# Kernel tuning notes

Hardware: AMD Instinct MI355X
Metric: run time of the kernel (lower is better)

Reference implementation:

```python
import jax, jax.numpy as jnp
import numpy as np

K = 2            # negative:positive edge ratio (init arg k)
N_NODES = 4096
N_EDGES = 8192
FEAT = 64


def setup_inputs() -> dict:
    key = jax.random.key(0)
    k1, k2, k3 = jax.random.split(key, 3)
    node_feature = jax.random.normal(k1, (N_NODES, FEAT), dtype=jnp.float32)
    edge_src = jax.random.randint(k2, (N_EDGES,), 0, N_NODES, dtype=jnp.int32)
    edge_dst = jax.random.randint(k3, (N_EDGES,), 0, N_NODES, dtype=jnp.int32)
    return {"node_feature": node_feature, "edge_src": edge_src, "edge_dst": edge_dst}


def reference(node_feature, edge_src, edge_dst):
    E = edge_src.shape[0]
    N = node_feature.shape[0]
    # [E, E] pairwise mask: candidate column j is valid for row i iff
    # dst[j] != dst[i] and dst[j] != src[i]
    valid = (edge_dst[:, None] != edge_dst[None, :]) & (edge_src[:, None] != edge_dst[None, :])
    # unsorted_segment_min over rows grouped by edge_src -> [N, E]
    segmin = jax.ops.segment_min(valid.astype(jnp.int8), edge_src, num_segments=N)
    # gather back per edge -> [E, E], flatten
    m = segmin[edge_src].reshape(-1).astype(bool)  # [E*E]
    num_negatives = jnp.sum(m)
    ratio = num_negatives // E                      # integer ratio as in TF code
    keep_prob = (K / ratio).astype(jnp.float32)
    u = jax.random.uniform(jax.random.key(42), (E * E,), dtype=jnp.float32)
    keep = m & (u < keep_prob)
    # fixed-size (jit-friendly) stand-in for tf.boolean_mask: expected count is K*E;
    # pad/truncate to exactly K*E kept flat indices (fill_value=0 pads).
    idx = jnp.nonzero(keep, size=K * E, fill_value=0)[0]
    rows = idx // E
    cols = idx % E
    edge_src_neg = edge_src[rows]
    edge_dst_neg = edge_dst[cols]
    return edge_src_neg, edge_dst_neg
```

## Files before the change

kernel.cpp:

```cpp
#include <hip/hip_runtime.h>
#include <stdint.h>
#include <math.h>

typedef unsigned int u32;
typedef unsigned long long u64;

#define E_CNT   8192
#define N_CNT   4096
#define TOT_N   (1u << 26)
#define OUT_K   16384
#define NODE_BM_WORDS 128
#define N_CHUNKS 1024

#define OFF_BAD      0x000000
#define OFF_CNT_DST  0x200000
#define OFF_CNT_SRC  0x204000
#define OFF_CCOUNT   0x208000
#define OFF_SCALARS  0x209000
#define OFF_KEEPBM   0x210000
#define ZERO_BYTES   0x209040

__device__ __forceinline__ u32 rotl32(u32 x, u32 d) {
  return __builtin_amdgcn_alignbit(x, x, 32u - d);
}

__device__ __forceinline__ void threefry2_0_42(u32 ia, u32 ib, u32& bits_a, u32& bits_b) {
  const u32 k1 = 42u, k2 = 0x1BD11BF0u;
  u32 a0 = ia + k1, a1r;
  u32 b0 = ib + k1;
  u32 A0 = 0u, A1 = a0;
  u32 B0 = 0u, B1 = b0;
#define R2(r) { A0 += A1; B0 += B1; A1 = rotl32(A1, r); B1 = rotl32(B1, r); A1 ^= A0; B1 ^= B0; }
  R2(13) R2(15) R2(26) R2(6)
  A0 += k1; B0 += k1; A1 += k2 + 1u; B1 += k2 + 1u;
  R2(17) R2(29) R2(16) R2(24)
  A0 += k2; B0 += k2; A1 += 2u; B1 += 2u;
  R2(13) R2(15) R2(26) R2(6)
   A1 += k1 + 3u; B1 += k1 + 3u;
  R2(17) R2(29) R2(16) R2(24)
  A0 += k1; B0 += k1; A1 += k2 + 4u; B1 += k2 + 4u;
  R2(13) R2(15) R2(26) R2(6)
  A0 += k2; B0 += k2; A1 += 5u; B1 += 5u;
#undef R2
  bits_a = A0 ^ A1;
  bits_b = B0 ^ B1;
  (void)a1r;
}

__global__ void k_build(const int* __restrict__ src, const int* __restrict__ dst,
                        u32* __restrict__ bad, u32* __restrict__ cnt_dst,
                        u32* __restrict__ cnt_src, int* __restrict__ out) {
  int tid = blockIdx.x * 256 + threadIdx.x;
  if (tid < N_CNT) {
    atomicOr(&bad[(u32)tid * NODE_BM_WORDS + ((u32)tid >> 5)], 1u << (tid & 31));
  }
  u32 s = (u32)src[tid], d = (u32)dst[tid];
  atomicOr(&bad[s * NODE_BM_WORDS + (d >> 5)], 1u << (d & 31));
  atomicAdd(&cnt_dst[d], 1u);
  atomicAdd(&cnt_src[s], 1u);
  int s0 = src[0], d0 = dst[0];
  out[tid] = s0;            out[tid + E_CNT] = s0;
  out[OUT_K + tid] = d0;    out[OUT_K + tid + E_CNT] = d0;
}

__global__ void __launch_bounds__(1024) k_rowcount(const u32* __restrict__ bad,
                                                   const u32* __restrict__ cnt_dst,
                                                   const u32* __restrict__ cnt_src,
                                                   u32* __restrict__ scal) {
  int wv = threadIdx.x >> 6, ln = threadIdx.x & 63;
  int n = blockIdx.x * 16 + wv;
  const u32* row = bad + (u32)n * NODE_BM_WORDS;
  u32 sum = 0;
#pragma unroll
  for (int h = 0; h < 2; ++h) {
    int w = ln + h * 64;
    u32 bits = row[w];
    while (bits) { int b = __ffs(bits) - 1; sum += cnt_dst[(w << 5) + b]; bits &= bits - 1; }
  }
#pragma unroll
  for (int off = 32; off > 0; off >>= 1) sum += __shfl_down(sum, off, 64);
  __shared__ u32 part[16];
  if (ln == 0) part[wv] = ((u32)E_CNT - sum) * cnt_src[n];
  __syncthreads();
  if (threadIdx.x == 0) {
    u32 tot = 0;
#pragma unroll
    for (int k = 0; k < 16; ++k) tot += part[k];
    atomicAdd(&scal[0], tot);
    __threadfence();
    if (atomicAdd(&scal[1], 1u) == 255u) {
      u32 nn = atomicAdd(&scal[0], 0u);
      u32 ratio = nn >> 13;
      float kp = 2.0f / (float)ratio;
      u32 T = (u32)ceil((double)kp * 8388608.0);
      u32 T9 = (T >= (1u << 23)) ? 0xFFFFFFFFu : (T << 9);
      atomicExch(&scal[2], T9);
    }
  }
}

__global__ void __launch_bounds__(256) k_sample(const int* __restrict__ src,
                                                const int* __restrict__ dst,
                                                const u32* __restrict__ bad,
                                                const u32* __restrict__ scal,
                                                u64* __restrict__ keep_bm,
                                                u32* __restrict__ ccount) {
  u32 wv = threadIdx.x >> 6, ln = threadIdx.x & 63;
  u32 i0w = blockIdx.x * 2048u + wv * 512u;
  u32 T9 = scal[2];
  u64 words[8];
  u64 any = 0;
#pragma unroll
  for (int j = 0; j < 4; ++j) {
    u32 ia = i0w + (u32)j * 128u + ln;
    u32 ba, bb;
    threefry2_0_42(ia, ia + 64u, ba, bb);
    u64 ma = __ballot(ba < T9);
    u64 mb = __ballot(bb < T9);
    words[2 * j] = ma; words[2 * j + 1] = mb;
    any |= ma | mb;
  }
  if (any) {
#pragma unroll
    for (int k = 0; k < 8; ++k) {
      if (words[k]) {
        u32 i = i0w + (u32)k * 64u + ln;
        bool kp = (words[k] >> ln) & 1ull;
        if (kp) {
          u32 n = (u32)src[i >> 13]; u32 v = (u32)dst[i & 8191];
          kp = ((bad[n * NODE_BM_WORDS + (v >> 5)] >> (v & 31)) & 1u) == 0u;
        }
        words[k] = __ballot(kp);
      }
    }
  }
  if (ln == 0) {
    u32 widx = i0w >> 6;
    ulonglong2* p = (ulonglong2*)&keep_bm[widx];
    p[0] = make_ulonglong2(words[0], words[1]);
    p[1] = make_ulonglong2(words[2], words[3]);
    p[2] = make_ulonglong2(words[4], words[5]);
    p[3] = make_ulonglong2(words[6], words[7]);
    u32 c = 0;
#pragma unroll
    for (int k = 0; k < 8; ++k) c += (u32)__popcll(words[k]);
    if (c) atomicAdd(&ccount[i0w >> 16], c);
  }
}

__global__ void k_compact(const int* __restrict__ src, const int* __restrict__ dst,
                          const u64* __restrict__ keep_bm, const u32* __restrict__ ccount,
                          int* __restrict__ out) {
  int c = blockIdx.x;
  int t = threadIdx.x;
  __shared__ u32 s[256];
  __shared__ u32 base_sh;

  u32 v[4]; u32 sum4 = 0;
#pragma unroll
  for (int k = 0; k < 4; ++k) { v[k] = ccount[4 * t + k]; sum4 += v[k]; }
  s[t] = sum4; __syncthreads();
  for (int off = 1; off < 256; off <<= 1) {
    u32 x = (t >= off) ? s[t - off] : 0u;
    __syncthreads();
    s[t] += x;
    __syncthreads();
  }
  if (t == (c >> 2)) {
    u32 excl = s[t] - sum4;
#pragma unroll
    for (int k = 0; k < 4; ++k) if (k < (c & 3)) excl += v[k];
    base_sh = excl;
  }
  __syncthreads();
  u32 coff_c = base_sh;
  __syncthreads();

  const u64* words = keep_bm + (size_t)c * 1024;
  u64 w[4];
  u32 cnt = 0;
#pragma unroll
  for (int k = 0; k < 4; ++k) { w[k] = words[4 * t + k]; cnt += (u32)__popcll(w[k]); }
  s[t] = cnt; __syncthreads();
  for (int off = 1; off < 256; off <<= 1) {
    u32 x = (t >= off) ? s[t - off] : 0u;
    __syncthreads();
    s[t] += x;
    __syncthreads();
  }
  u32 rank = coff_c + s[t] - cnt;
  u32 tbase = (u32)c * 65536u + (u32)t * 256u;
#pragma unroll
  for (int k = 0; k < 4; ++k) {
    u64 bits = w[k];
    while (bits) {
      int b = __ffsll((unsigned long long)bits) - 1;
      if (rank < OUT_K) {
        u32 tt = tbase + (u32)k * 64u + (u32)b;
        out[rank]         = src[tt >> 13];
        out[OUT_K + rank] = dst[tt & 8191];
      }
      rank++;
      bits &= bits - 1;
    }
  }
}

extern "C" void kernel_launch(void* const* d_in, const int* in_sizes, int n_in,
                              void* d_out, int out_size, void* d_ws, size_t ws_size,
                              hipStream_t stream) {
  const int* src = (const int*)d_in[1];
  const int* dst = (const int*)d_in[2];
  int* out = (int*)d_out;
  char* ws = (char*)d_ws;

  u32* bad     = (u32*)(ws + OFF_BAD);
  u32* cnt_dst = (u32*)(ws + OFF_CNT_DST);
  u32* cnt_src = (u32*)(ws + OFF_CNT_SRC);
  u32* ccount  = (u32*)(ws + OFF_CCOUNT);
  u32* scal    = (u32*)(ws + OFF_SCALARS);
  u64* keep_bm = (u64*)(ws + OFF_KEEPBM);

  hipMemsetAsync(ws, 0, ZERO_BYTES, stream);
  k_build<<<E_CNT / 256, 256, 0, stream>>>(src, dst, bad, cnt_dst, cnt_src, out);
  k_rowcount<<<N_CNT / 16, 1024, 0, stream>>>(bad, cnt_dst, cnt_src, scal);
  k_sample<<<TOT_N / 2048, 256, 0, stream>>>(src, dst, bad, scal, keep_bm, ccount);
  k_compact<<<N_CHUNKS, 256, 0, stream>>>(src, dst, keep_bm, ccount, out);
}
```

Before: 189.8 us.

## Interleave four threefry streams and replace shared-memory scans with wave shuffles

The sampling kernel now evaluates four independent threefry counters per call instead of two. This gives the scheduler more independent integer work to hide ALU latency, at the cost of more live registers. The compaction kernel replaces two 256-wide shared-memory Hillis-Steele scans, each with many barriers, with a masked reduction of chunk counts plus wave-level shuffle scans that need a single barrier. The mask and shuffle logic must reproduce the same exclusive offsets for the output to stay correct.

```diff
diff --git a/kernel.cpp b/kernel.cpp
--- a/kernel.cpp
+++ b/kernel.cpp
@@ -24,27 +24,36 @@
   return __builtin_amdgcn_alignbit(x, x, 32u - d);
 }
 
-__device__ __forceinline__ void threefry2_0_42(u32 ia, u32 ib, u32& bits_a, u32& bits_b) {
+__device__ __forceinline__ void threefry4_0_42(u32 ia, u32 ib, u32 ic, u32 id,
+                                               u32& ra, u32& rb, u32& rc, u32& rd) {
   const u32 k1 = 42u, k2 = 0x1BD11BF0u;
-  u32 a0 = ia + k1, a1r;
-  u32 b0 = ib + k1;
-  u32 A0 = 0u, A1 = a0;
-  u32 B0 = 0u, B1 = b0;
-#define R2(r) { A0 += A1; B0 += B1; A1 = rotl32(A1, r); B1 = rotl32(B1, r); A1 ^= A0; B1 ^= B0; }
-  R2(13) R2(15) R2(26) R2(6)
-  A0 += k1; B0 += k1; A1 += k2 + 1u; B1 += k2 + 1u;
-  R2(17) R2(29) R2(16) R2(24)
-  A0 += k2; B0 += k2; A1 += 2u; B1 += 2u;
-  R2(13) R2(15) R2(26) R2(6)
-   A1 += k1 + 3u; B1 += k1 + 3u;
-  R2(17) R2(29) R2(16) R2(24)
-  A0 += k1; B0 += k1; A1 += k2 + 4u; B1 += k2 + 4u;
-  R2(13) R2(15) R2(26) R2(6)
-  A0 += k2; B0 += k2; A1 += 5u; B1 += 5u;
-#undef R2
-  bits_a = A0 ^ A1;
-  bits_b = B0 ^ B1;
-  (void)a1r;
+  u32 A0 = 0u, A1 = ia + k1;
+  u32 B0 = 0u, B1 = ib + k1;
+  u32 C0 = 0u, C1 = ic + k1;
+  u32 D0 = 0u, D1 = id + k1;
+#define R4(r) { A0 += A1; B0 += B1; C0 += C1; D0 += D1; \
+  A1 = rotl32(A1, r); B1 = rotl32(B1, r); C1 = rotl32(C1, r); D1 = rotl32(D1, r); \
+  A1 ^= A0; B1 ^= B0; C1 ^= C0; D1 ^= D0; }
+#define INJ(c0, c1) { A0 += (c0); B0 += (c0); C0 += (c0); D0 += (c0); \
+  A1 += (c1); B1 += (c1); C1 += (c1); D1 += (c1); }
+#define INJ1(c1) { A1 += (c1); B1 += (c1); C1 += (c1); D1 += (c1); }
+  R4(13) R4(15) R4(26) R4(6)
+  INJ(k1, k2 + 1u)
+  R4(17) R4(29) R4(16) R4(24)
+  INJ(k2, 2u)
+  R4(13) R4(15) R4(26) R4(6)
+  INJ1(k1 + 3u)
+  R4(17) R4(29) R4(16) R4(24)
+  INJ(k1, k2 + 4u)
+  R4(13) R4(15) R4(26) R4(6)
+  INJ(k2, 5u)
+#undef R4
+#undef INJ
+#undef INJ1
+  ra = A0 ^ A1;
+  rb = B0 ^ B1;
+  rc = C0 ^ C1;
+  rd = D0 ^ D1;
 }
 
 __global__ void k_build(const int* __restrict__ src, const int* __restrict__ dst,
@@ -111,14 +120,19 @@
   u64 words[8];
   u64 any = 0;
 #pragma unroll
-  for (int j = 0; j < 4; ++j) {
-    u32 ia = i0w + (u32)j * 128u + ln;
-    u32 ba, bb;
-    threefry2_0_42(ia, ia + 64u, ba, bb);
-    u64 ma = __ballot(ba < T9);
-    u64 mb = __ballot(bb < T9);
-    words[2 * j] = ma; words[2 * j + 1] = mb;
-    any |= ma | mb;
+  for (int h = 0; h < 2; ++h) {
+    u32 i0 = i0w + (u32)h * 256u + ln;
+    u32 b0, b1, b2, b3;
+    threefry4_0_42(i0, i0 + 64u, i0 + 128u, i0 + 192u, b0, b1, b2, b3);
+    u64 m0 = __ballot(b0 < T9);
+    u64 m1 = __ballot(b1 < T9);
+    u64 m2 = __ballot(b2 < T9);
+    u64 m3 = __ballot(b3 < T9);
+    words[4 * h]     = m0;
+    words[4 * h + 1] = m1;
+    words[4 * h + 2] = m2;
+    words[4 * h + 3] = m3;
+    any |= m0 | m1 | m2 | m3;
   }
   if (any) {
 #pragma unroll
@@ -153,42 +167,42 @@
                           int* __restrict__ out) {
   int c = blockIdx.x;
   int t = threadIdx.x;
-  __shared__ u32 s[256];
-  __shared__ u32 base_sh;
-
-  u32 v[4]; u32 sum4 = 0;
-#pragma unroll
-  for (int k = 0; k < 4; ++k) { v[k] = ccount[4 * t + k]; sum4 += v[k]; }
-  s[t] = sum4; __syncthreads();
-  for (int off = 1; off < 256; off <<= 1) {
-    u32 x = (t >= off) ? s[t - off] : 0u;
-    __syncthreads();
-    s[t] += x;
-    __syncthreads();
-  }
-  if (t == (c >> 2)) {
-    u32 excl = s[t] - sum4;
-#pragma unroll
-    for (int k = 0; k < 4; ++k) if (k < (c & 3)) excl += v[k];
-    base_sh = excl;
-  }
-  __syncthreads();
-  u32 coff_c = base_sh;
-  __syncthreads();
+  int wvid = t >> 6, ln = t & 63;
+  __shared__ u32 red[4];
+  __shared__ u32 wsum[4];
+
+  u32 part = 0;
+#pragma unroll
+  for (int k = 0; k < 4; ++k) {
+    int q = t + k * 256;
+    u32 vq = ccount[q];
+    part += (q < c) ? vq : 0u;
+  }
+  u32 r = part;
+#pragma unroll
+  for (int off = 32; off > 0; off >>= 1) r += __shfl_down(r, off, 64);
+  if (ln == 0) red[wvid] = r;
 
   const u64* words = keep_bm + (size_t)c * 1024;
   u64 w[4];
   u32 cnt = 0;
 #pragma unroll
   for (int k = 0; k < 4; ++k) { w[k] = words[4 * t + k]; cnt += (u32)__popcll(w[k]); }
-  s[t] = cnt; __syncthreads();
-  for (int off = 1; off < 256; off <<= 1) {
-    u32 x = (t >= off) ? s[t - off] : 0u;
-    __syncthreads();
-    s[t] += x;
-    __syncthreads();
-  }
-  u32 rank = coff_c + s[t] - cnt;
+
+  u32 scan = cnt;
+#pragma unroll
+  for (int off = 1; off < 64; off <<= 1) {
+    u32 x = __shfl_up(scan, off, 64);
+    if (ln >= off) scan += x;
+  }
+  if (ln == 63) wsum[wvid] = scan;
+  __syncthreads();
+  u32 coff_c = red[0] + red[1] + red[2] + red[3];
+  u32 wbase = 0;
+#pragma unroll
+  for (int k = 0; k < 4; ++k) wbase += (k < wvid) ? wsum[k] : 0u;
+
+  u32 rank = coff_c + wbase + scan - cnt;
   u32 tbase = (u32)c * 65536u + (u32)t * 256u;
 #pragma unroll
   for (int k = 0; k < 4; ++k) {
```

Measured after the change: 187.2 us. About the same (-1.4%).
